# Optimization experiments

Hardware: AMD Instinct MI355X
Metric: run time of the kernel (lower is better)

Reference implementation:

```python
import jax, jax.numpy as jnp
import numpy as np
from jax import lax

B, CIN, CV, H, W = 2, 256, 128, 96, 320
NS, K, PAD = 8, 3, 1
HID = 4 * CV
EPS = 1e-5

def _ffn_shapes(p):
    return {p+'_g': (CV,), p+'_b': (CV,), p+'_w1': (CV, HID), p+'_b1': (HID,),
            p+'_dw': (HID, 1, 3, 3), p+'_bdw': (HID,), p+'_w2': (HID, CV), p+'_b2': (CV,)}

def _win_shapes(p):
    return {p+'_g': (CV,), p+'_b': (CV,), p+'_wq': (CV, CV), p+'_wk': (CV, CV),
            p+'_wv': (CV, CV), p+'_wo': (CV, CV), p+'_bo': (CV,)}

PARAM_SHAPES = {'agg_w1': (CIN, CIN // 2), 'agg_b1': (CIN // 2,), 'agg_w2': (CIN // 2, CV), 'agg_b2': (CV,),
                'ol_g': (CV,), 'ol_b': (CV,), 'ol_wv': (CV, CV), 'ol_wa': (CV, K ** 4), 'ol_ba': (K ** 4,),
                'ol_wo': (CV, CV), 'ol_bo': (CV,)}
PARAM_SHAPES.update(_ffn_shapes('f1')); PARAM_SHAPES.update(_win_shapes('w'))
PARAM_SHAPES.update(_ffn_shapes('f2')); PARAM_SHAPES.update(_win_shapes('s'))
PARAM_SHAPES.update(_ffn_shapes('f3'))
PNAMES = list(PARAM_SHAPES.keys())


def ln(x, g, b):
    mu = x.mean(-1, keepdims=True)
    var = ((x - mu) ** 2).mean(-1, keepdims=True)
    return (x - mu) * lax.rsqrt(var + EPS) * g + b


def sink_softmax(logits):
    # softmax with an implicit extra zero-logit 'sink' slot (sink competition):
    # probs = exp(l) / (sum(exp(l)) + exp(0)), computed stably.
    m = jnp.maximum(logits.max(-1, keepdims=True), 0.0)
    e = jnp.exp(logits - m)
    return e / (e.sum(-1, keepdims=True) + jnp.exp(-m))


def outlook_attn(x, g, b, wv, wa, ba, wo, bo):
    # VOLO-style outlook attention, kernel K, stride 1, padding PAD (pool is identity at stride 1)
    Bb, Hh, Ww, C = x.shape
    xn = ln(x, g, b)
    v = xn @ wv                                                     # B,H,W,C
    vp = jnp.pad(v, ((0, 0), (PAD, PAD), (PAD, PAD), (0, 0)))
    patches = jnp.stack([vp[:, i:i + Hh, j:j + Ww, :] for i in range(K) for j in range(K)], axis=3)  # B,H,W,K*K,C
    attn = (xn @ wa + ba).reshape(Bb, Hh, Ww, K * K, K * K)
    attn = sink_softmax(attn)
    out = jnp.einsum('bhwpq,bhwqc->bhwpc', attn, patches)           # B,H,W,K*K,C
    acc = jnp.zeros_like(vp)                                        # fold (overlap-add)
    idx = 0
    for i in range(K):
        for j in range(K):
            acc = acc.at[:, i:i + Hh, j:j + Ww, :].add(out[:, :, :, idx, :])
            idx += 1
    y = acc[:, PAD:PAD + Hh, PAD:PAD + Ww, :]
    return y @ wo + bo


def swin_mask(Hh, Ww, wh, ww):
    # standard swin shifted-window cross-region mask, built statically
    sh, sw = wh // 2, ww // 2
    img = np.zeros((Hh, Ww), np.int32)
    cnt = 0
    for hs in (slice(0, -wh), slice(-wh, -sh), slice(-sh, None)):
        for ws in (slice(0, -ww), slice(-ww, -sw), slice(-sw, None)):
            img[hs, ws] = cnt; cnt += 1
    win = img.reshape(Hh // wh, wh, Ww // ww, ww).transpose(0, 2, 1, 3).reshape(-1, wh * ww)
    mask = np.where(win[:, :, None] != win[:, None, :], -100.0, 0.0).astype(np.float32)
    return jnp.asarray(mask)  # [NS*NS, L, L]


def window_attn(x, g, b, wq, wk, wv, wo, bo, with_shift):
    Bb, Hh, Ww, C = x.shape
    wh, ww = Hh // NS, Ww // NS
    xn = ln(x, g, b)
    if with_shift:
        xn = jnp.roll(xn, (-(wh // 2), -(ww // 2)), axis=(1, 2))

    def part(t):  # -> [B, NS*NS, wh*ww, C]
        return t.reshape(Bb, NS, wh, NS, ww, C).transpose(0, 1, 3, 2, 4, 5).reshape(Bb, NS * NS, wh * ww, C)

    q, k, v = part(xn @ wq), part(xn @ wk), part(xn @ wv)
    scores = jnp.einsum('bnqc,bnkc->bnqk', q, k) / jnp.sqrt(jnp.asarray(C, x.dtype))
    if with_shift:
        scores = scores + swin_mask(Hh, Ww, wh, ww)[None]
    out = jnp.einsum('bnqk,bnkc->bnqc', sink_softmax(scores), v)
    out = out.reshape(Bb, NS, NS, wh, ww, C).transpose(0, 1, 3, 2, 4, 5).reshape(Bb, Hh, Ww, C)
    if with_shift:
        out = jnp.roll(out, (wh // 2, ww // 2), axis=(1, 2))
    return out @ wo + bo


def conv_ffn(x, g, b, w1, b1, dw, bdw, w2, b2):
    # pre-norm conv FFN: 1x1 expand -> depthwise 3x3 -> GELU -> 1x1 project
    xn = ln(x, g, b)
    h = (xn @ w1 + b1).transpose(0, 3, 1, 2)                        # B,HID,H,W
    h = lax.conv_general_dilated(h, dw, (1, 1), 'SAME', feature_group_count=HID)
    h = h + bdw[None, :, None, None]
    h = jax.nn.gelu(h, approximate=False).transpose(0, 2, 3, 1)
    return h @ w2 + b2


def pos_embed(Bb, Hh, Ww, nf, dtype):
    # DETR-style normalized 2D sine/cosine positional embedding, nf feats per axis
    scale = 2.0 * np.pi
    eps = 1e-6
    ye = jnp.arange(1, Hh + 1, dtype=jnp.float32); ye = ye / (ye[-1] + eps) * scale
    xe = jnp.arange(1, Ww + 1, dtype=jnp.float32); xe = xe / (xe[-1] + eps) * scale
    dim_t = 10000.0 ** (2.0 * (jnp.arange(nf) // 2) / nf)

    def emb(p):  # [N] -> [N, nf]
        t = p[:, None] / dim_t
        return jnp.stack([jnp.sin(t[:, 0::2]), jnp.cos(t[:, 1::2])], axis=2).reshape(p.shape[0], -1)

    py, px = emb(ye), emb(xe)
    pos = jnp.concatenate([jnp.broadcast_to(py[:, None, :], (Hh, Ww, nf)),
                           jnp.broadcast_to(px[None, :, :], (Hh, Ww, nf))], axis=-1)
    return jnp.broadcast_to(pos[None], (Bb, Hh, Ww, 2 * nf)).astype(dtype)


def forward(x, p):
    f = x.transpose(0, 2, 3, 1)                                     # B,H,W,CIN
    f = jax.nn.relu(f @ p['agg_w1'] + p['agg_b1'])                  # channels_agg (BN folded, eval)
    f = f @ p['agg_w2'] + p['agg_b2']                               # B,H,W,CV
    f = f + outlook_attn(f, p['ol_g'], p['ol_b'], p['ol_wv'], p['ol_wa'], p['ol_ba'], p['ol_wo'], p['ol_bo'])
    f = f + conv_ffn(f, p['f1_g'], p['f1_b'], p['f1_w1'], p['f1_b1'], p['f1_dw'], p['f1_bdw'], p['f1_w2'], p['f1_b2'])
    f = f + pos_embed(f.shape[0], f.shape[1], f.shape[2], CV // 2, f.dtype)
    f = f + window_attn(f, p['w_g'], p['w_b'], p['w_wq'], p['w_wk'], p['w_wv'], p['w_wo'], p['w_bo'], False)
    f = f + conv_ffn(f, p['f2_g'], p['f2_b'], p['f2_w1'], p['f2_b1'], p['f2_dw'], p['f2_bdw'], p['f2_w2'], p['f2_b2'])
    f = f + window_attn(f, p['s_g'], p['s_b'], p['s_wq'], p['s_wk'], p['s_wv'], p['s_wo'], p['s_bo'], True)
    f = f + conv_ffn(f, p['f3_g'], p['f3_b'], p['f3_w1'], p['f3_b1'], p['f3_dw'], p['f3_bdw'], p['f3_w2'], p['f3_b2'])
    return f.transpose(0, 3, 1, 2)                                  # B,CV,H,W


def setup_inputs():
    keys = iter(jax.random.split(jax.random.key(0), 64))
    inp = {'x': jax.random.normal(next(keys), (B, CIN, H, W), jnp.float32)}
    for name, shp in PARAM_SHAPES.items():
        if name.endswith('_g'):
            inp[name] = jnp.ones(shp, jnp.float32)
        elif len(shp) == 1:
            inp[name] = jnp.zeros(shp, jnp.float32)
        else:
            inp[name] = jax.random.normal(next(keys), shp, jnp.float32) * 0.02
    return inp


def reference(x, agg_w1, agg_b1, agg_w2, agg_b2, ol_g, ol_b, ol_wv, ol_wa, ol_ba, ol_wo, ol_bo,
              f1_g, f1_b, f1_w1, f1_b1, f1_dw, f1_bdw, f1_w2, f1_b2,
              w_g, w_b, w_wq, w_wk, w_wv, w_wo, w_bo,
              f2_g, f2_b, f2_w1, f2_b1, f2_dw, f2_bdw, f2_w2, f2_b2,
              s_g, s_b, s_wq, s_wk, s_wv, s_wo, s_bo,
              f3_g, f3_b, f3_w1, f3_b1, f3_dw, f3_bdw, f3_w2, f3_b2):
    _l = locals()
    p = {k: _l[k] for k in PNAMES}
    return forward(x, p)
```

## Files before the change

### kernel.cpp

```cpp
#include <hip/hip_runtime.h>

typedef __bf16 bf16;
typedef __bf16 bf16x8 __attribute__((ext_vector_type(8)));
typedef __bf16 bf16x4 __attribute__((ext_vector_type(4)));
typedef float  f32x4  __attribute__((ext_vector_type(4)));

#define MFMA_BF16(a, b, c) __builtin_amdgcn_mfma_f32_16x16x32_bf16(a, b, c, 0, 0, 0)

constexpr int cB    = 2;
constexpr int cH    = 96;
constexpr int cW    = 320;
constexpr int cC    = 128;
constexpr int cNPIX = cH * cW;
constexpr int cNTOK = cB * cNPIX;
constexpr int cAS   = 84;

struct WJob  { const float* src; bf16* dst; int K; int M; };
struct WJobs { WJob j[19]; };

__global__ __launch_bounds__(256) void k_wt(WJobs jobs)
{
    __shared__ float tile[32][33];
    const WJob jb = jobs.j[blockIdx.z];
    int k0 = blockIdx.y * 32, m0 = blockIdx.x * 32;
    if (k0 >= jb.K || m0 >= jb.M) return;
    int tx = threadIdx.x, ty = threadIdx.y;
#pragma unroll
    for (int i = 0; i < 32; i += 8) {
        int kk = k0 + ty + i, mm = m0 + tx;
        tile[ty + i][tx] = (kk < jb.K && mm < jb.M) ? jb.src[(size_t)kk * jb.M + mm] : 0.f;
    }
    __syncthreads();
#pragma unroll
    for (int i = 0; i < 32; i += 8) {
        int mm = m0 + ty + i, kk = k0 + tx;
        if (mm < jb.M && kk < jb.K)
            jb.dst[(size_t)mm * jb.K + kk] = (bf16)tile[tx][ty + i];
    }
}

__global__ __launch_bounds__(256) void k_dwt(const float* s0, const float* s1, const float* s2,
                                             float* d0, float* d1, float* d2)
{
    const float* s = blockIdx.x == 0 ? s0 : (blockIdx.x == 1 ? s1 : s2);
    float*       d = blockIdx.x == 0 ? d0 : (blockIdx.x == 1 ? d1 : d2);
    for (int i = threadIdx.x; i < 512 * 9; i += 256) {
        int c = i / 9, tap = i - c * 9;
        d[tap * 512 + c] = s[i];
    }
}

__global__ __launch_bounds__(256) void k_postab(float* __restrict__ yt, float* __restrict__ xt)
{
    int i = blockIdx.x * 256 + threadIdx.x;
    const float TWO_PI = 6.283185307179586f;
    const float KSC = -9.210340371976184f / 32.f;
    if (i < 96 * 64) {
        int h = i >> 6, c = i & 63;
        float p = (float)(h + 1) * (TWO_PI / (96.f + 1e-6f));
        float val = p * expf((float)(c >> 1) * KSC);
        yt[i] = (c & 1) ? cosf(val) : sinf(val);
    }
    if (i < 320 * 64) {
        int w = i >> 6, c = i & 63;
        float p = (float)(w + 1) * (TWO_PI / (320.f + 1e-6f));
        float val = p * expf((float)(c >> 1) * KSC);
        xt[i] = (c & 1) ? cosf(val) : sinf(val);
    }
}

__global__ __launch_bounds__(256) void k_chw2hwc(const float* __restrict__ in,
                                                 bf16* __restrict__ out)
{
    __shared__ float tile[32][33];
    const int Cc = 256;
    int s0 = blockIdx.x * 32;
    int c0 = blockIdx.y * 32;
    int b  = blockIdx.z;
    const float* ip = in  + (size_t)b * Cc * cNPIX;
    bf16*        op = out + (size_t)b * cNPIX * Cc;
    int tx = threadIdx.x, ty = threadIdx.y;
#pragma unroll
    for (int i = 0; i < 32; i += 8)
        tile[ty + i][tx] = ip[(size_t)(c0 + ty + i) * cNPIX + s0 + tx];
    __syncthreads();
#pragma unroll
    for (int i = 0; i < 32; i += 8)
        op[(size_t)(s0 + ty + i) * Cc + c0 + tx] = (bf16)tile[tx][ty + i];
}

template<int QKVS>
__global__ __launch_bounds__(256) void k_gemm128(const bf16* __restrict__ A,
                                                 const bf16* __restrict__ Wt,
                                                 const float* __restrict__ bias,
                                                 bf16* __restrict__ outB, int M,
                                                 bf16* __restrict__ vtb,
                                                 bf16* __restrict__ ksb)
{
    __shared__ bf16 As[128][136];
    __shared__ bf16 Sb[64][136];

    const int NS = M >> 7;
    const int l  = blockIdx.x;
    const int r8 = l % (8 * NS);
    const int qq = l / (8 * NS);
    const int bm = (qq * 8 + (r8 & 7)) * 128;
    const int bn = (r8 >> 3) * 128;

    const int t = threadIdx.x;
    const int lane = t & 63, wid = t >> 6;
    const int wm = (wid >> 1) * 64, wn = (wid & 1) * 64;
    const int lr = lane & 15, lg = lane >> 4;

    const bf16* wp = Wt + (size_t)(bn + wn + lr) * 128 + lg * 8;
    bf16x8 bwA[4], bwB[4];
#pragma unroll
    for (int nf = 0; nf < 4; ++nf)
        bwA[nf] = *(const bf16x8*)(wp + (size_t)(nf * 16) * 128);

#pragma unroll
    for (int i = 0; i < 8; ++i) {
        int o = i * 256 + t;
        int row = o >> 4, cg = (o & 15) * 8;
        *(bf16x8*)&As[row][cg] = *(const bf16x8*)(A + (size_t)(bm + row) * 128 + cg);
    }
    __syncthreads();

    const f32x4 zero4 = {0.f, 0.f, 0.f, 0.f};
    f32x4 acc[4][4];
#pragma unroll
    for (int i = 0; i < 4; ++i)
#pragma unroll
        for (int j = 0; j < 4; ++j) acc[i][j] = zero4;

#pragma unroll
    for (int ks = 0; ks < 4; ++ks) {
        const bf16x8* cur = (ks & 1) ? bwB : bwA;
        bf16x8*       nxt = (ks & 1) ? bwA : bwB;
        if (ks < 3) {
#pragma unroll
            for (int nf = 0; nf < 4; ++nf)
                nxt[nf] = *(const bf16x8*)(wp + (size_t)(nf * 16) * 128 + (ks + 1) * 32);
        }
        bf16x8 af[4];
#pragma unroll
        for (int mf = 0; mf < 4; ++mf)
            af[mf] = *(const bf16x8*)&As[wm + mf*16 + lr][ks*32 + lg*8];
        __builtin_amdgcn_s_setprio(1);
#pragma unroll
        for (int mf = 0; mf < 4; ++mf)
#pragma unroll
            for (int nf = 0; nf < 4; ++nf)
                acc[mf][nf] = MFMA_BF16(af[mf], cur[nf], acc[mf][nf]);
        __builtin_amdgcn_s_setprio(0);
    }

    const bool vpart = (QKVS >= 0) && (bn == 256);
    const bool kpart = (QKVS >= 0) && (bn == 128);
    if (!vpart) {
#pragma unroll
        for (int half = 0; half < 2; ++half) {
            __syncthreads();
            if ((wid >> 1) == half) {
#pragma unroll
                for (int nf = 0; nf < 4; ++nf) {
                    int col = wn + nf * 16 + lr;
                    float bv = bias ? bias[bn + col] : 0.f;
#pragma unroll
                    for (int mf = 0; mf < 4; ++mf)
#pragma unroll
                        for (int r = 0; r < 4; ++r)
                            Sb[mf * 16 + lg * 4 + r][col] = (bf16)(acc[mf][nf][r] + bv);
                }
            }
            __syncthreads();
            if (!kpart) {
                const int ldo = (QKVS >= 0) ? 128 : M;
#pragma unroll
                for (int i = 0; i < 4; ++i) {
                    int o = i * 256 + t;
                    int row = o >> 4, cg = (o & 15) * 8;
                    *(bf16x8*)(outB + (size_t)(bm + half * 64 + row) * ldo + bn + cg) =
                        *(const bf16x8*)&Sb[row][cg];
                }
            } else {
#pragma unroll
                for (int i = 0; i < 4; ++i) {
                    int o = i * 256 + t;
                    int row = o >> 4, cg = (o & 15) * 8;
                    int gt = bm + half * 64 + row;
                    int b_ = gt / cNPIX, hw = gt - b_ * cNPIX;
                    int h = hw / cW, w = hw - (hw / cW) * cW;
                    int h0 = (QKVS == 1) ? ((h + 90) % 96)  : h;
                    int w0 = (QKVS == 1) ? ((w + 300) % 320) : w;
                    int nh = h0 / 12, kh = h0 - nh * 12;
                    int nw = w0 / 40, kw = w0 - nw * 40;
                    size_t krow = (size_t)((b_ * 64 + nh * 8 + nw) * 480 + kh * 40 + kw);
                    *(bf16x8*)(ksb + krow * 128 + cg) = *(const bf16x8*)&Sb[row][cg];
                }
            }
        }
    } else {
        const int lr_ = t & 15, cg_ = t >> 4;
        const int gt = bm + lr_ * 8;
        const int b_ = gt / cNPIX, hw = gt % cNPIX;
        const int h = hw / cW, w = hw % cW;
        const int h0 = (QKVS == 1) ? ((h + 90) % 96) : h;
        const int nh = h0 / 12, kh = h0 - nh * 12;
#pragma unroll
        for (int cp = 0; cp < 2; ++cp) {
            __syncthreads();
            if ((wid & 1) == cp) {
#pragma unroll
                for (int nf = 0; nf < 4; ++nf) {
                    int cl = nf * 16 + lr;
#pragma unroll
                    for (int mf = 0; mf < 4; ++mf)
#pragma unroll
                        for (int r = 0; r < 4; ++r)
                            Sb[cl][wm + mf * 16 + lg * 4 + r] = (bf16)acc[mf][nf][r];
                }
            }
            __syncthreads();
#pragma unroll
            for (int i = 0; i < 4; ++i) {
                int chl = cg_ + 16 * i;
                int ch  = cp * 64 + chl;
                bf16x8 e = *(const bf16x8*)&Sb[chl][lr_ * 8];
#pragma unroll
                for (int hi = 0; hi < 2; ++hi) {
                    int wv = (QKVS == 1) ? ((w + hi * 4 + 300) % 320) : (w + hi * 4);
                    int nw = wv / 40, kw = wv - nw * 40;
                    bf16* dst = vtb + ((size_t)((b_ * 64 + nh * 8 + nw) * 128 + ch)) * 480 + kh * 40 + kw;
                    bf16x4 hv;
#pragma unroll
                    for (int j = 0; j < 4; ++j) hv[j] = e[hi * 4 + j];
                    *(bf16x4*)dst = hv;
                }
            }
        }
    }
}

__global__ __launch_bounds__(256) void k_gemm128_wa(const bf16* __restrict__ A,
                                                    const bf16* __restrict__ Wt,
                                                    const float* __restrict__ bias,
                                                    bf16* __restrict__ outA)
{
    __shared__ bf16 As[128][136];
    __shared__ bf16 Sb[64][88];

    const int bm = blockIdx.x * 128;
    const int t = threadIdx.x;
    const int lane = t & 63, wid = t >> 6;
    const int wm = (wid >> 1) * 64, wn = (wid & 1) * 64;
    const int lr = lane & 15, lg = lane >> 4;

    bf16x8 zrow;
#pragma unroll
    for (int j = 0; j < 8; ++j) zrow[j] = (bf16)0.f;

    bool okc[4];
    const bf16* wp = Wt + (size_t)(wn + lr) * 128 + lg * 8;
#pragma unroll
    for (int nf = 0; nf < 4; ++nf) okc[nf] = (wn + nf * 16 + lr) < 81;

    bf16x8 bwA[4], bwB[4];
#pragma unroll
    for (int nf = 0; nf < 4; ++nf)
        bwA[nf] = okc[nf] ? *(const bf16x8*)(wp + (size_t)(nf * 16) * 128) : zrow;

#pragma unroll
    for (int i = 0; i < 8; ++i) {
        int o = i * 256 + t;
        int row = o >> 4, cg = (o & 15) * 8;
        *(bf16x8*)&As[row][cg] = *(const bf16x8*)(A + (size_t)(bm + row) * 128 + cg);
    }
    __syncthreads();

    const f32x4 zero4 = {0.f, 0.f, 0.f, 0.f};
    f32x4 acc[4][4];
#pragma unroll
    for (int i = 0; i < 4; ++i)
#pragma unroll
        for (int j = 0; j < 4; ++j) acc[i][j] = zero4;

#pragma unroll
    for (int ks = 0; ks < 4; ++ks) {
        const bf16x8* cur = (ks & 1) ? bwB : bwA;
        bf16x8*       nxt = (ks & 1) ? bwA : bwB;
        if (ks < 3) {
#pragma unroll
            for (int nf = 0; nf < 4; ++nf)
                nxt[nf] = okc[nf] ? *(const bf16x8*)(wp + (size_t)(nf * 16) * 128 + (ks + 1) * 32) : zrow;
        }
        bf16x8 af[4];
#pragma unroll
        for (int mf = 0; mf < 4; ++mf)
            af[mf] = *(const bf16x8*)&As[wm + mf*16 + lr][ks*32 + lg*8];
        __builtin_amdgcn_s_setprio(1);
#pragma unroll
        for (int mf = 0; mf < 4; ++mf)
#pragma unroll
            for (int nf = 0; nf < 4; ++nf)
                acc[mf][nf] = MFMA_BF16(af[mf], cur[nf], acc[mf][nf]);
        __builtin_amdgcn_s_setprio(0);
    }

#pragma unroll
    for (int half = 0; half < 2; ++half) {
        __syncthreads();
        if ((wid >> 1) == half) {
#pragma unroll
            for (int nf = 0; nf < 4; ++nf) {
                int col = wn + nf * 16 + lr;
                if (col >= 84) continue;
                float bv = (col < 81) ? bias[col] : 0.f;
#pragma unroll
                for (int mf = 0; mf < 4; ++mf)
#pragma unroll
                    for (int r = 0; r < 4; ++r) {
                        float vv = (col < 81) ? (acc[mf][nf][r] + bv) : 0.f;
                        Sb[mf * 16 + lg * 4 + r][col] = (bf16)vv;
                    }
            }
        }
        __syncthreads();
#pragma unroll
        for (int i = 0; i < 6; ++i) {
            int o = i * 256 + t;
            if (o < 64 * 21) {
                int row = o / 21, cq = (o - row * 21) * 4;
                *(bf16x4*)(outA + (size_t)(bm + half * 64 + row) * cAS + cq) =
                    *(const bf16x4*)&Sb[row][cq];
            }
        }
    }
}

template<bool OUTBF, bool RELU, bool RES, bool POS, bool LNOUT, bool TOUT>
__global__ __launch_bounds__(256) void k_gemm_res(const bf16* __restrict__ A,
                                                  const bf16* __restrict__ Wt,
                                                  const float* __restrict__ bias,
                                                  const float* __restrict__ res,
                                                  float* __restrict__ outF,
                                                  bf16* __restrict__ outB,
                                                  int K,
                                                  const float* __restrict__ ytab,
                                                  const float* __restrict__ xtab,
                                                  const float* __restrict__ lng,
                                                  const float* __restrict__ lnb,
                                                  bf16* __restrict__ xnbO)
{
    __shared__ bf16 As[128][40];
    __shared__ bf16 Bs[128][40];
    __shared__ float Sf[64][136];

    const int bm = blockIdx.x * 128;
    const int t = threadIdx.x;
    const int lane = t & 63, wid = t >> 6;
    const int wm = (wid >> 1) * 64, wn = (wid & 1) * 64;
    const int lr = lane & 15, lg = lane >> 4;

    const f32x4 zero4 = {0.f, 0.f, 0.f, 0.f};
    f32x4 acc[4][4];
#pragma unroll
    for (int i = 0; i < 4; ++i)
#pragma unroll
        for (int j = 0; j < 4; ++j) acc[i][j] = zero4;

    for (int k0 = 0; k0 < K; k0 += 32) {
#pragma unroll
        for (int i = 0; i < 2; ++i) {
            int idx = t + i * 256;
            int row = idx >> 2, kg = (idx & 3) * 8;
            *(bf16x8*)&As[row][kg] = *(const bf16x8*)(A + (size_t)(bm + row) * K + k0 + kg);
            *(bf16x8*)&Bs[row][kg] = *(const bf16x8*)(Wt + (size_t)row * K + k0 + kg);
        }
        __syncthreads();
        bf16x8 af[4], bf[4];
#pragma unroll
        for (int mf = 0; mf < 4; ++mf)
            af[mf] = *(const bf16x8*)&As[wm + mf*16 + lr][lg * 8];
#pragma unroll
        for (int nf = 0; nf < 4; ++nf)
            bf[nf] = *(const bf16x8*)&Bs[wn + nf*16 + lr][lg * 8];
        __builtin_amdgcn_s_setprio(1);
#pragma unroll
        for (int mf = 0; mf < 4; ++mf)
#pragma unroll
            for (int nf = 0; nf < 4; ++nf)
                acc[mf][nf] = MFMA_BF16(af[mf], bf[nf], acc[mf][nf]);
        __builtin_amdgcn_s_setprio(0);
        __syncthreads();
    }

    if (OUTBF) {
        bf16 (*Sb)[136] = (bf16(*)[136])Sf;
#pragma unroll
        for (int nf = 0; nf < 4; ++nf) {
            int col = wn + nf * 16 + lr;
            float bv = bias ? bias[col] : 0.f;
#pragma unroll
            for (int mf = 0; mf < 4; ++mf)
#pragma unroll
                for (int r = 0; r < 4; ++r) {
                    float vv = acc[mf][nf][r] + bv;
                    if (RELU) vv = fmaxf(vv, 0.f);
                    Sb[wm + mf * 16 + lg * 4 + r][col] = (bf16)vv;
                }
        }
        __syncthreads();
#pragma unroll
        for (int i = 0; i < 8; ++i) {
            int o = i * 256 + t;
            int row = o >> 4, cg = (o & 15) * 8;
            *(bf16x8*)(outB + (size_t)(bm + row) * 128 + cg) = *(const bf16x8*)&Sb[row][cg];
        }
    } else {
        const int b_   = bm / cNPIX;
        const int hw0  = bm - b_ * cNPIX;
        for (int half = 0; half < 2; ++half) {
            __syncthreads();
            if ((wid >> 1) == half) {
#pragma unroll
                for (int nf = 0; nf < 4; ++nf) {
                    int col = wn + nf * 16 + lr;
                    float bv = bias ? bias[col] : 0.f;
#pragma unroll
                    for (int mf = 0; mf < 4; ++mf)
#pragma unroll
                        for (int r = 0; r < 4; ++r)
                            Sf[mf * 16 + lg * 4 + r][col] = acc[mf][nf][r] + bv;
                }
            }
            __syncthreads();
            if (!TOUT) {
#pragma unroll
                for (int i = 0; i < 8; ++i) {
                    int o = i * 256 + t;
                    int row = o >> 5, cq = (o & 31) * 4;
                    int grow = bm + half * 64 + row;
                    float4 v = *(const float4*)&Sf[row][cq];
                    if (POS) {
                        int hw = grow % cNPIX;
                        int h = hw / cW, w = hw - (hw / cW) * cW;
                        float4 p = (cq < 64) ? *(const float4*)(ytab + (h << 6) + cq)
                                             : *(const float4*)(xtab + (w << 6) + cq - 64);
                        v.x += p.x; v.y += p.y; v.z += p.z; v.w += p.w;
                    }
                    if (RES) {
                        float4 rr = *(const float4*)(res + (size_t)grow * 128 + cq);
                        v.x += rr.x; v.y += rr.y; v.z += rr.z; v.w += rr.w;
                    }
                    if (LNOUT) {
                        float s  = v.x + v.y + v.z + v.w;
                        float sq = v.x*v.x + v.y*v.y + v.z*v.z + v.w*v.w;
#pragma unroll
                        for (int mk = 1; mk < 32; mk <<= 1) {
                            s  += __shfl_xor(s,  mk);
                            sq += __shfl_xor(sq, mk);
                        }
                        float mu = s * (1.f / 128.f);
                        float rs = rsqrtf(sq * (1.f / 128.f) - mu * mu + 1e-5f);
                        float4 g4 = *(const float4*)(lng + cq);
                        float4 b4 = *(const float4*)(lnb + cq);
                        bf16x4 xo;
                        xo[0] = (bf16)((v.x - mu) * rs * g4.x + b4.x);
                        xo[1] = (bf16)((v.y - mu) * rs * g4.y + b4.y);
                        xo[2] = (bf16)((v.z - mu) * rs * g4.z + b4.z);
                        xo[3] = (bf16)((v.w - mu) * rs * g4.w + b4.w);
                        *(bf16x4*)(xnbO + (size_t)grow * 128 + cq) = xo;
                    }
                    *(float4*)(outF + (size_t)grow * 128 + cq) = v;
                }
            } else {
#pragma unroll
                for (int i = 0; i < 8; ++i) {
                    int o = i * 256 + t;
                    int row = o >> 5, cq = (o & 31) * 4;
                    int grow = bm + half * 64 + row;
                    float4 v = *(const float4*)&Sf[row][cq];
                    float4 rr = *(const float4*)(res + (size_t)grow * 128 + cq);
                    v.x += rr.x; v.y += rr.y; v.z += rr.z; v.w += rr.w;
                    *(float4*)&Sf[row][cq] = v;
                }
                __syncthreads();
                const int lane16 = t & 15;
#pragma unroll
                for (int p = 0; p < 8; ++p) {
                    int col = p * 16 + (t >> 4);
                    float4 v;
                    v.x = Sf[lane16 * 4 + 0][col];
                    v.y = Sf[lane16 * 4 + 1][col];
                    v.z = Sf[lane16 * 4 + 2][col];
                    v.w = Sf[lane16 * 4 + 3][col];
                    *(float4*)(outF + ((size_t)(b_ * 128 + col)) * cNPIX
                               + hw0 + half * 64 + lane16 * 4) = v;
                }
            }
        }
    }
}

__global__ __launch_bounds__(256) void k_olk_gather(const bf16* __restrict__ v,
                                                    const bf16* __restrict__ attn,
                                                    bf16* __restrict__ y)
{
    __shared__ bf16  Ls[100][136];
    __shared__ float pr[16][84];
    __shared__ float coef[16][26];

    const int t  = threadIdx.x;
    const int px = t >> 4;
    const int j  = t & 15;
    const int pix0 = blockIdx.x * 16;
    const int b   = pix0 / cNPIX;
    const int hw0 = pix0 % cNPIX;
    const int h   = hw0 / cW, w0 = hw0 % cW;
    const int pix = pix0 + px;
    const int w   = w0 + px;

    const size_t bbase = (size_t)b * cNPIX;

    for (int e = px; e < 100; e += 16) {
        const int a  = e / 20, cc = e - a * 20;
        const int sh = h + a - 2, sw = w0 + cc - 2;
        bf16x8 val;
        if ((unsigned)sh < (unsigned)cH && (unsigned)sw < (unsigned)cW) {
            val = *(const bf16x8*)(v + (bbase + (size_t)sh * cW + sw) * 128 + j * 8);
        } else {
#pragma unroll
            for (int q = 0; q < 8; ++q) val[q] = (bf16)0.f;
        }
        *(bf16x8*)&Ls[e][j * 8] = val;
    }

    if (j < 9) {
        const int p  = j;
        const int pi = p / 3, pj = p - pi * 3;
        const int hh = h + 1 - pi, ww = w + 1 - pj;
        float prv[9];
        if ((unsigned)hh < (unsigned)cH && (unsigned)ww < (unsigned)cW) {
            const size_t row = (size_t)(bbase + (size_t)hh * cW + ww);
            const bf16* arow = attn + row * cAS + p * 9;
            float lg[9];
            float m = 0.f;
#pragma unroll
            for (int q = 0; q < 9; ++q) { lg[q] = (float)arow[q]; m = fmaxf(m, lg[q]); }
            float se = 0.f;
#pragma unroll
            for (int q = 0; q < 9; ++q) { prv[q] = __expf(lg[q] - m); se += prv[q]; }
            float inv = 1.f / (se + __expf(-m));
#pragma unroll
            for (int q = 0; q < 9; ++q) prv[q] *= inv;
        } else {
#pragma unroll
            for (int q = 0; q < 9; ++q) prv[q] = 0.f;
        }
#pragma unroll
        for (int q = 0; q < 9; ++q) pr[px][p * 9 + q] = prv[q];
    }
    __syncthreads();

    for (int d = j; d < 25; d += 16) {
        const int a  = d / 5, bb = d - a * 5;
        float s = 0.f;
#pragma unroll
        for (int pi = 0; pi < 3; ++pi) {
            const int qi = pi + a - 2;
            if ((unsigned)qi >= 3u) continue;
#pragma unroll
            for (int pj = 0; pj < 3; ++pj) {
                const int qj = pj + bb - 2;
                if ((unsigned)qj >= 3u) continue;
                s += pr[px][(pi * 3 + pj) * 9 + qi * 3 + qj];
            }
        }
        coef[px][d] = s;
    }
    __syncthreads();

    float acc[8] = {};
#pragma unroll
    for (int a = 0; a < 5; ++a) {
#pragma unroll
        for (int bb = 0; bb < 5; ++bb) {
            const float cf = coef[px][a * 5 + bb];
            const bf16x8 v8 = *(const bf16x8*)&Ls[a * 20 + px + bb][j * 8];
#pragma unroll
            for (int e = 0; e < 8; ++e) acc[e] = fmaf(cf, (float)v8[e], acc[e]);
        }
    }
    bf16x8 o8;
#pragma unroll
    for (int e = 0; e < 8; ++e) o8[e] = (bf16)acc[e];
    *(bf16x8*)(y + (size_t)pix * 128 + j * 8) = o8;
}

__global__ __launch_bounds__(256) void k_dwconv_gelu(const bf16* __restrict__ h1,
                                                     const float* __restrict__ dwt,
                                                     const float* __restrict__ bdw,
                                                     bf16* __restrict__ h2)
{
    const int t   = threadIdx.x;
    const int c2  = t * 2;
    const int blk = blockIdx.x;
    const int row = blk >> 4;
    const int seg = blk & 15;
    const int bb  = row / cH, h = row % cH;
    const int w0  = seg * 20;

    float2 wgt[9];
#pragma unroll
    for (int k = 0; k < 9; ++k)
        wgt[k] = *(const float2*)(dwt + k * 512 + c2);
    if (h == 0) {
        wgt[0].x = wgt[0].y = wgt[1].x = wgt[1].y = wgt[2].x = wgt[2].y = 0.f;
    }
    if (h == cH - 1) {
        wgt[6].x = wgt[6].y = wgt[7].x = wgt[7].y = wgt[8].x = wgt[8].y = 0.f;
    }
    const float2 bias = *(const float2*)(bdw + c2);

    const size_t base = (size_t)bb * cNPIX;
    const int hm = (h == 0) ? 0 : h - 1;
    const int hp = (h == cH - 1) ? h : h + 1;
    const bf16* rp0 = h1 + (base + (size_t)hm * cW + w0) * 512 + c2;
    const bf16* rp1 = h1 + (base + (size_t)h  * cW + w0) * 512 + c2;
    const bf16* rp2 = h1 + (base + (size_t)hp * cW + w0) * 512 + c2;

    auto ldc = [&](const bf16* rp, int wofs) -> float2 {
        unsigned u = *(const unsigned*)(rp + (size_t)wofs * 512);
        float2 r;
        r.x = __uint_as_float(u << 16);
        r.y = __uint_as_float(u & 0xffff0000u);
        return r;
    };
    auto gelu = [](float x) -> float {
        float x2 = x * x;
        float z2 = fmaf(x2 * x, 0.0713548162726f, 1.5957691216057308f * x);
        float t1 = 1.f / (1.f + __expf(-z2));
        return x * t1;
    };

    float2 cm[3], c0[3], cp[3];
    if (seg == 0) {
#pragma unroll
        for (int r = 0; r < 3; ++r) { cm[r].x = 0.f; cm[r].y = 0.f; }
    } else {
        cm[0] = ldc(rp0, -1); cm[1] = ldc(rp1, -1); cm[2] = ldc(rp2, -1);
    }
    c0[0] = ldc(rp0, 0); c0[1] = ldc(rp1, 0); c0[2] = ldc(rp2, 0);

    bf16* op = h2 + (base + (size_t)h * cW + w0) * 512 + c2;

    for (int j = 0; j < 20; ++j) {
        if (j == 19 && seg == 15) {
#pragma unroll
            for (int r = 0; r < 3; ++r) { cp[r].x = 0.f; cp[r].y = 0.f; }
        } else {
            cp[0] = ldc(rp0, j + 1); cp[1] = ldc(rp1, j + 1); cp[2] = ldc(rp2, j + 1);
        }
        float a0 = bias.x, a1 = bias.y;
#pragma unroll
        for (int r = 0; r < 3; ++r) {
            a0 = fmaf(cm[r].x, wgt[r * 3 + 0].x, a0);
            a1 = fmaf(cm[r].y, wgt[r * 3 + 0].y, a1);
            a0 = fmaf(c0[r].x, wgt[r * 3 + 1].x, a0);
            a1 = fmaf(c0[r].y, wgt[r * 3 + 1].y, a1);
            a0 = fmaf(cp[r].x, wgt[r * 3 + 2].x, a0);
            a1 = fmaf(cp[r].y, wgt[r * 3 + 2].y, a1);
        }
        a0 = gelu(a0);
        a1 = gelu(a1);
        union { bf16 hh[2]; unsigned int u; } o2;
        o2.hh[0] = (bf16)a0;
        o2.hh[1] = (bf16)a1;
        *(unsigned int*)(op + (size_t)j * 512) = o2.u;
#pragma unroll
        for (int r = 0; r < 3; ++r) { cm[r] = c0[r]; c0[r] = cp[r]; }
    }
}

template<bool SHIFT>
__global__ __launch_bounds__(512) void k_win_attn(const bf16* __restrict__ q,
                                                  const bf16* __restrict__ ks,
                                                  const bf16* __restrict__ vt,
                                                  bf16* __restrict__ out)
{
    __shared__ bf16 Ks[2][32][136];
    __shared__ bf16 Vs[2][128][44];
    __shared__ bf16 Ps[8][16][44];

    const int t = threadIdx.x, lane = t & 63, wid = t >> 6;
    const int lr = lane & 15, lg = lane >> 4;
    const int wb = blockIdx.x;
    const int b  = wb >> 6, win = wb & 63;
    const int nh = win >> 3, nw = win & 7;
    const int qbase = blockIdx.y * 128 + wid * 16;

    const float SCALE   = 0.088388347648318447f;
    const float MASKRAW = 100.f / 0.088388347648318447f;

    auto tokOf = [&](int p) {
        int ph = nh * 12 + p / 40;
        int pw = nw * 40 + (p % 40);
        if (SHIFT) {
            ph += 6;  if (ph >= cH) ph -= cH;
            pw += 20; if (pw >= cW) pw -= cW;
        }
        return b * cNPIX + ph * cW + pw;
    };

    int qp = min(qbase + lr, 479);
    const bf16* qptr = q + (size_t)tokOf(qp) * 128;
    bf16x8 qf[4];
#pragma unroll
    for (int c = 0; c < 4; ++c)
        qf[c] = *(const bf16x8*)(qptr + c * 32 + lg * 8);

    int labq[4];
    if (SHIFT) {
#pragma unroll
        for (int r = 0; r < 4; ++r) {
            int qrow = min(qbase + lg * 4 + r, 479);
            int qr = qrow / 40, qc = qrow - qr * 40;
            int rh = (nh == 7) ? (qr < 6 ? 1 : 2) : 0;
            int rc = (nw == 7) ? (qc < 20 ? 1 : 2) : 0;
            labq[r] = rh * 3 + rc;
        }
    }

    const bf16* kbase = ks + (size_t)wb * 480 * 128;
    const bf16* vbase = vt + (size_t)wb * 128 * 480;
    auto loadK = [&](int kt) {
        return *(const bf16x8*)(kbase + (size_t)(kt * 32 + (t >> 4)) * 128 + (t & 15) * 8);
    };
    auto loadV = [&](int kt) {
        return *(const bf16x8*)(vbase + (size_t)(t >> 2) * 480 + kt * 32 + (t & 3) * 8);
    };

    bf16x8 kreg = loadK(0);
    bf16x8 vreg = loadV(0);
    *(bf16x8*)&Ks[0][t >> 4][(t & 15) * 8] = kreg;
    *(bf16x8*)&Vs[0][t >> 2][(t & 3) * 8]  = vreg;
    kreg = loadK(1);
    vreg = loadV(1);

    int kc0 = lr, kr0 = 0;
    int kc1 = 16 + lr, kr1 = 0;

    const f32x4 zero4 = {0.f, 0.f, 0.f, 0.f};
    float m_run[4] = {0.f, 0.f, 0.f, 0.f};
    float mguard = 8.f;
    f32x4 l4 = zero4;
    f32x4 o[8];
#pragma unroll
    for (int nf = 0; nf < 8; ++nf) o[nf] = zero4;

    bf16x8 ones8;
#pragma unroll
    for (int j = 0; j < 8; ++j) ones8[j] = (bf16)1.f;

    for (int kt = 0; kt < 15; ++kt) {
        const int cur = kt & 1;
        __syncthreads();
        if (kt + 1 < 15) {
            *(bf16x8*)&Ks[cur ^ 1][t >> 4][(t & 15) * 8] = kreg;
            *(bf16x8*)&Vs[cur ^ 1][t >> 2][(t & 3) * 8]  = vreg;
            if (kt + 2 < 15) {
                kreg = loadK(kt + 2);
                vreg = loadV(kt + 2);
            }
        }

        f32x4 s0 = zero4, s1 = zero4;
        __builtin_amdgcn_s_setprio(1);
#pragma unroll
        for (int c = 0; c < 4; ++c) {
            bf16x8 kf0 = *(const bf16x8*)&Ks[cur][lr][c * 32 + lg * 8];
            bf16x8 kf1 = *(const bf16x8*)&Ks[cur][16 + lr][c * 32 + lg * 8];
            s0 = MFMA_BF16(qf[c], kf0, s0);
            s1 = MFMA_BF16(qf[c], kf1, s1);
        }
        __builtin_amdgcn_s_setprio(0);

        if (SHIFT) {
            int rh0 = (nh == 7) ? (kr0 < 6 ? 1 : 2) : 0;
            int rc0 = (nw == 7) ? (kc0 < 20 ? 1 : 2) : 0;
            int rh1 = (nh == 7) ? (kr1 < 6 ? 1 : 2) : 0;
            int rc1 = (nw == 7) ? (kc1 < 20 ? 1 : 2) : 0;
            int lab0 = rh0 * 3 + rc0;
            int lab1 = rh1 * 3 + rc1;
#pragma unroll
            for (int r = 0; r < 4; ++r) {
                if (labq[r] != lab0) s0[r] -= MASKRAW;
                if (labq[r] != lab1) s1[r] -= MASKRAW;
            }
        }
        kc0 += 32; if (kc0 >= 40) { kc0 -= 40; ++kr0; }
        kc1 += 32; if (kc1 >= 40) { kc1 -= 40; ++kr1; }

        float tm = fmaxf(fmaxf(fmaxf(s0[0], s0[1]), fmaxf(s0[2], s0[3])),
                         fmaxf(fmaxf(s1[0], s1[1]), fmaxf(s1[2], s1[3])));
        if (__any(tm * SCALE > mguard)) {
#pragma unroll
            for (int r = 0; r < 4; ++r) {
                float mx = fmaxf(s0[r], s1[r]);
#pragma unroll
                for (int off = 1; off < 16; off <<= 1) mx = fmaxf(mx, __shfl_xor(mx, off));
                float nm = fmaxf(m_run[r], mx * SCALE);
                float sc = __expf(m_run[r] - nm);
#pragma unroll
                for (int nf = 0; nf < 8; ++nf) o[nf][r] *= sc;
                l4[r] *= sc;
                m_run[r] = nm;
            }
            mguard = fminf(fminf(m_run[0], m_run[1]), fminf(m_run[2], m_run[3])) + 8.f;
        }

#pragma unroll
        for (int r = 0; r < 4; ++r) {
            float p0 = __expf(fmaf(s0[r], SCALE, -m_run[r]));
            float p1 = __expf(fmaf(s1[r], SCALE, -m_run[r]));
            Ps[wid][lg * 4 + r][lr]      = (bf16)p0;
            Ps[wid][lg * 4 + r][16 + lr] = (bf16)p1;
        }

        bf16x8 pa = *(const bf16x8*)&Ps[wid][lr][lg * 8];
        __builtin_amdgcn_s_setprio(1);
        l4 = MFMA_BF16(pa, ones8, l4);
#pragma unroll
        for (int nf = 0; nf < 8; ++nf) {
            bf16x8 bv = *(const bf16x8*)&Vs[cur][nf * 16 + lr][lg * 8];
            o[nf] = MFMA_BF16(pa, bv, o[nf]);
        }
        __builtin_amdgcn_s_setprio(0);
    }

#pragma unroll
    for (int r = 0; r < 4; ++r) {
        int qrow = qbase + lg * 4 + r;
        if (qrow >= 480) continue;
        float inv = 1.f / (l4[r] + __expf(-m_run[r]));
        size_t ooff = (size_t)tokOf(qrow) * 128;
#pragma unroll
        for (int nf = 0; nf < 8; ++nf)
            out[ooff + nf * 16 + lr] = (bf16)(o[nf][r] * inv);
    }
}

extern "C" void kernel_launch(void* const* d_in, const int* in_sizes, int n_in,
                              void* d_out, int out_size, void* d_ws, size_t ws_size,
                              hipStream_t stream)
{
    (void)in_sizes; (void)n_in; (void)out_size; (void)ws_size;

    const float* X = (const float*)d_in[0];

    char* ws = (char*)d_ws;
    float* f    = (float*)ws;                                 ws += (size_t)cNTOK * 128 * 4;
    bf16*  xnb  = (bf16*)ws;                                  ws += (size_t)cNTOK * 128 * 2;
    bf16*  bufA = (bf16*)ws;                                  ws += (size_t)cNTOK * 512 * 2;
    bf16*  bufB = (bf16*)ws;                                  ws += (size_t)cNTOK * 512 * 2;
    bf16*  wts  = (bf16*)ws;

    size_t wo_off = 0;
    auto nextw = [&](int K, int M) { bf16* p = wts + wo_off; wo_off += (size_t)K * M; return p; };
    bf16* agg_w1t = nextw(256, 128);
    bf16* agg_w2t = nextw(128, 128);
    bf16* ol_wvt  = nextw(128, 128);
    bf16* ol_wat  = nextw(128, 81);
    bf16* ol_wot  = nextw(128, 128);
    bf16* f1_w1t  = nextw(128, 512);
    bf16* f1_w2t  = nextw(512, 128);
    bf16* w_qkvt  = nextw(128, 384);
    bf16* w_wot   = nextw(128, 128);
    bf16* f2_w1t  = nextw(128, 512);
    bf16* f2_w2t  = nextw(512, 128);
    bf16* s_qkvt  = nextw(128, 384);
    bf16* s_wot   = nextw(128, 128);
    bf16* f3_w1t  = nextw(128, 512);
    bf16* f3_w2t  = nextw(512, 128);
    float* dwt1 = (float*)(wts + wo_off);
    float* dwt2 = dwt1 + 512 * 9;
    float* dwt3 = dwt2 + 512 * 9;
    float* ytab = dwt3 + 512 * 9;
    float* xtab = ytab + 96 * 64;

    WJobs jobs;
    int ji = 0;
    auto addj = [&](int src_idx, bf16* dst, int K, int M) {
        jobs.j[ji++] = WJob{(const float*)d_in[src_idx], dst, K, M};
    };
    addj(1,  agg_w1t, 256, 128);
    addj(3,  agg_w2t, 128, 128);
    addj(7,  ol_wvt,  128, 128);
    addj(8,  ol_wat,  128, 81);
    addj(10, ol_wot,  128, 128);
    addj(14, f1_w1t,  128, 512);
    addj(18, f1_w2t,  512, 128);
    addj(22, w_qkvt,           128, 128);
    addj(23, w_qkvt + 128*128, 128, 128);
    addj(24, w_qkvt + 256*128, 128, 128);
    addj(25, w_wot,   128, 128);
    addj(29, f2_w1t,  128, 512);
    addj(33, f2_w2t,  512, 128);
    addj(37, s_qkvt,           128, 128);
    addj(38, s_qkvt + 128*128, 128, 128);
    addj(39, s_qkvt + 256*128, 128, 128);
    addj(40, s_wot,   128, 128);
    addj(44, f3_w1t,  128, 512);
    addj(48, f3_w2t,  512, 128);
    k_wt<<<dim3(16, 16, 19), dim3(32, 8), 0, stream>>>(jobs);
    k_dwt<<<3, 256, 0, stream>>>((const float*)d_in[16], (const float*)d_in[31],
                                 (const float*)d_in[46], dwt1, dwt2, dwt3);
    k_postab<<<80, 256, 0, stream>>>(ytab, xtab);

    const int nTT = cNTOK / 128;

    k_chw2hwc<<<dim3(cNPIX / 32, 256 / 32, cB), dim3(32, 8), 0, stream>>>(X, bufA);
    k_gemm_res<true, true, false, false, false, false><<<nTT, 256, 0, stream>>>(
        bufA, agg_w1t, (const float*)d_in[2], nullptr, nullptr, bufB, 256,
        nullptr, nullptr, nullptr, nullptr, nullptr);
    k_gemm_res<false, false, false, false, true, false><<<nTT, 256, 0, stream>>>(
        bufB, agg_w2t, (const float*)d_in[4], nullptr, f, nullptr, 128,
        nullptr, nullptr, (const float*)d_in[5], (const float*)d_in[6], xnb);

    {
        bf16*  vb   = bufA;
        bf16*  gout = bufA + (size_t)cNTOK * 128;
        bf16*  atn  = bufB;
        k_gemm128<-1><<<nTT, 256, 0, stream>>>(xnb, ol_wvt, nullptr, vb, 128, nullptr, nullptr);
        k_gemm128_wa<<<nTT, 256, 0, stream>>>(xnb, ol_wat, (const float*)d_in[9], atn);
        k_olk_gather<<<cNTOK / 16, 256, 0, stream>>>(vb, atn, gout);
        k_gemm_res<false, false, true, false, true, false><<<nTT, 256, 0, stream>>>(
            gout, ol_wot, (const float*)d_in[11], f, f, nullptr, 128,
            nullptr, nullptr, (const float*)d_in[12], (const float*)d_in[13], xnb);
    }

    auto run_ffn = [&](int base, bf16* w1t, bf16* w2t, float* dwt, bool pos,
                       const float* lnG, const float* lnB, float* outT) {
        k_gemm128<-1><<<nTT * 4, 256, 0, stream>>>(
            xnb, w1t, (const float*)d_in[base + 3], bufA, 512, nullptr, nullptr);
        k_dwconv_gelu<<<cB * cH * 16, 256, 0, stream>>>(
            bufA, dwt, (const float*)d_in[base + 5], bufB);
        if (pos) {
            k_gemm_res<false, false, true, true, true, false><<<nTT, 256, 0, stream>>>(
                bufB, w2t, (const float*)d_in[base + 7], f, f, nullptr, 512,
                ytab, xtab, lnG, lnB, xnb);
        } else if (lnG) {
            k_gemm_res<false, false, true, false, true, false><<<nTT, 256, 0, stream>>>(
                bufB, w2t, (const float*)d_in[base + 7], f, f, nullptr, 512,
                nullptr, nullptr, lnG, lnB, xnb);
        } else {
            k_gemm_res<false, false, true, false, false, true><<<nTT, 256, 0, stream>>>(
                bufB, w2t, (const float*)d_in[base + 7], f, outT, nullptr, 512,
                nullptr, nullptr, nullptr, nullptr, nullptr);
        }
    };

    auto run_win = [&](int base, bf16* qkvt, bf16* wot, bool shift,
                       const float* lnG, const float* lnB) {
        bf16* qb  = bufA;
        bf16* ksb = bufA + (size_t)cNTOK * 128;
        bf16* vtb = bufA + (size_t)cNTOK * 256;
        bf16* ao  = bufB;
        if (shift)
            k_gemm128<1><<<nTT * 3, 256, 0, stream>>>(xnb, qkvt, nullptr, qb, 384, vtb, ksb);
        else
            k_gemm128<0><<<nTT * 3, 256, 0, stream>>>(xnb, qkvt, nullptr, qb, 384, vtb, ksb);
        if (shift) k_win_attn<true ><<<dim3(128, 4), 512, 0, stream>>>(qb, ksb, vtb, ao);
        else       k_win_attn<false><<<dim3(128, 4), 512, 0, stream>>>(qb, ksb, vtb, ao);
        k_gemm_res<false, false, true, false, true, false><<<nTT, 256, 0, stream>>>(
            ao, wot, (const float*)d_in[base + 6], f, f, nullptr, 128,
            nullptr, nullptr, lnG, lnB, xnb);
    };

    run_ffn(12, f1_w1t, f1_w2t, dwt1, true,
            (const float*)d_in[20], (const float*)d_in[21], nullptr);
    run_win(20, w_qkvt, w_wot, false,
            (const float*)d_in[27], (const float*)d_in[28]);
    run_ffn(27, f2_w1t, f2_w2t, dwt2, false,
            (const float*)d_in[35], (const float*)d_in[36], nullptr);
    run_win(35, s_qkvt, s_wot, true,
            (const float*)d_in[42], (const float*)d_in[43]);
    run_ffn(42, f3_w1t, f3_w2t, dwt3, false, nullptr, nullptr,
            (float*)d_out);
}
```

Measured before the change: 540.0 us.

## Double-buffer shared tiles with register prefetch in residual GEMM kernel

```diff
diff --git a/kernel.cpp b/kernel.cpp
--- a/kernel.cpp
+++ b/kernel.cpp
@@ -352,8 +352,8 @@
                                                   const float* __restrict__ lnb,
                                                   bf16* __restrict__ xnbO)
 {
-    __shared__ bf16 As[128][40];
-    __shared__ bf16 Bs[128][40];
+    __shared__ bf16 As[2][128][40];
+    __shared__ bf16 Bs[2][128][40];
     __shared__ float Sf[64][136];
 
     const int bm = blockIdx.x * 128;
@@ -362,6 +362,26 @@
     const int wm = (wid >> 1) * 64, wn = (wid & 1) * 64;
     const int lr = lane & 15, lg = lane >> 4;
 
+    const int r0 = t >> 2,          kg0 = (t & 3) * 8;
+    const int r1 = (t + 256) >> 2,  kg1 = ((t + 256) & 3) * 8;
+
+    const int nks = K >> 5;
+
+    auto loadAW = [&](int k0, bf16x8* ra, bf16x8* rw) {
+        ra[0] = *(const bf16x8*)(A  + (size_t)(bm + r0) * K + k0 + kg0);
+        ra[1] = *(const bf16x8*)(A  + (size_t)(bm + r1) * K + k0 + kg1);
+        rw[0] = *(const bf16x8*)(Wt + (size_t)r0 * K + k0 + kg0);
+        rw[1] = *(const bf16x8*)(Wt + (size_t)r1 * K + k0 + kg1);
+    };
+
+    bf16x8 ra[2], rw[2];
+    loadAW(0, ra, rw);
+    *(bf16x8*)&As[0][r0][kg0] = ra[0];
+    *(bf16x8*)&As[0][r1][kg1] = ra[1];
+    *(bf16x8*)&Bs[0][r0][kg0] = rw[0];
+    *(bf16x8*)&Bs[0][r1][kg1] = rw[1];
+    if (nks > 1) loadAW(32, ra, rw);
+
     const f32x4 zero4 = {0.f, 0.f, 0.f, 0.f};
     f32x4 acc[4][4];
 #pragma unroll
@@ -369,22 +389,23 @@
 #pragma unroll
         for (int j = 0; j < 4; ++j) acc[i][j] = zero4;
 
-    for (int k0 = 0; k0 < K; k0 += 32) {
-#pragma unroll
-        for (int i = 0; i < 2; ++i) {
-            int idx = t + i * 256;
-            int row = idx >> 2, kg = (idx & 3) * 8;
-            *(bf16x8*)&As[row][kg] = *(const bf16x8*)(A + (size_t)(bm + row) * K + k0 + kg);
-            *(bf16x8*)&Bs[row][kg] = *(const bf16x8*)(Wt + (size_t)row * K + k0 + kg);
-        }
+    for (int ks = 0; ks < nks; ++ks) {
+        const int cur = ks & 1;
         __syncthreads();
+        if (ks + 1 < nks) {
+            *(bf16x8*)&As[cur ^ 1][r0][kg0] = ra[0];
+            *(bf16x8*)&As[cur ^ 1][r1][kg1] = ra[1];
+            *(bf16x8*)&Bs[cur ^ 1][r0][kg0] = rw[0];
+            *(bf16x8*)&Bs[cur ^ 1][r1][kg1] = rw[1];
+            if (ks + 2 < nks) loadAW((ks + 2) * 32, ra, rw);
+        }
         bf16x8 af[4], bf[4];
 #pragma unroll
         for (int mf = 0; mf < 4; ++mf)
-            af[mf] = *(const bf16x8*)&As[wm + mf*16 + lr][lg * 8];
+            af[mf] = *(const bf16x8*)&As[cur][wm + mf*16 + lr][lg * 8];
 #pragma unroll
         for (int nf = 0; nf < 4; ++nf)
-            bf[nf] = *(const bf16x8*)&Bs[wn + nf*16 + lr][lg * 8];
+            bf[nf] = *(const bf16x8*)&Bs[cur][wn + nf*16 + lr][lg * 8];
         __builtin_amdgcn_s_setprio(1);
 #pragma unroll
         for (int mf = 0; mf < 4; ++mf)
@@ -392,8 +413,8 @@
             for (int nf = 0; nf < 4; ++nf)
                 acc[mf][nf] = MFMA_BF16(af[mf], bf[nf], acc[mf][nf]);
         __builtin_amdgcn_s_setprio(0);
-        __syncthreads();
-    }
+    }
+    __syncthreads();
 
     if (OUTBF) {
         bf16 (*Sb)[136] = (bf16(*)[136])Sf;
```

New measurement: 528.7 us. 1.02x faster.
